# Optimization experiments

Hardware: AMD Instinct MI355X
Metric: run time of the kernel (lower is better)

The kernel has to match this reference:

```python
import jax, jax.numpy as jnp
import numpy as np

B, SQ, SK, E, H = 2, 256, 512, 512, 256

def _lin_init(k, fan_in, fan_out):
    return jax.random.normal(k, (fan_in, fan_out), jnp.float32) / np.sqrt(fan_in)

def setup_inputs() -> dict:
    key = jax.random.key(0)
    ks = jax.random.split(key, 16)
    inp = {
        'query': jax.random.normal(ks[0], (B, SQ, E), jnp.float32),
        'key':   jax.random.normal(ks[1], (B, SK, E), jnp.float32),
        # encoders
        'Wqe': _lin_init(ks[2], E, H), 'bqe': jnp.zeros((H,), jnp.float32),
        'Wke': _lin_init(ks[3], E, H), 'bke': jnp.zeros((H,), jnp.float32),
        # importance predictor: Linear(2H,H) x1, Linear(H,H) x2, Linear(H,1)
        'W0': _lin_init(ks[4], 2 * H, H), 'b0': jnp.zeros((H,), jnp.float32),
        'W1': _lin_init(ks[5], H, H),     'b1': jnp.zeros((H,), jnp.float32),
        'W2': _lin_init(ks[6], H, H),     'b2': jnp.zeros((H,), jnp.float32),
        'Wf': _lin_init(ks[7], H, 1),     'bf': jnp.zeros((1,), jnp.float32),
        # variance estimator: Linear(2H,H), Linear(H,1), Softplus
        'Wv1': _lin_init(ks[8], 2 * H, H), 'bv1': jnp.zeros((H,), jnp.float32),
        'Wv2': _lin_init(ks[9], H, 1),     'bv2': jnp.zeros((1,), jnp.float32),
    }
    return inp

def reference(query, key, Wqe, bqe, Wke, bke, W0, b0, W1, b1, W2, b2, Wf, bf, Wv1, bv1, Wv2, bv2):
    # Encoders (dropout is identity at eval): [B,Sq,H] and [B,Sk,H]
    qf = jax.nn.relu(jnp.einsum('bqe,eh->bqh', query, Wqe) + bqe)
    kf = jax.nn.relu(jnp.einsum('bke,eh->bkh', key, Wke) + bke)

    # concat([qf, kf]) @ W == qf @ W[:H] + kf @ W[H:]; avoid materializing the 2H concat
    Hd = qf.shape[-1]
    # importance predictor, layer 0 over all (q,k) pairs -> [B,Sq,Sk,H]
    q_part = jnp.einsum('bqh,hd->bqd', qf, W0[:Hd])
    k_part = jnp.einsum('bkh,hd->bkd', kf, W0[Hd:])
    h = jax.nn.relu(q_part[:, :, None, :] + k_part[:, None, :, :] + b0)
    h = jax.nn.relu(jnp.einsum('bqkh,hd->bqkd', h, W1) + b1)
    h = jax.nn.relu(jnp.einsum('bqkh,hd->bqkd', h, W2) + b2)
    importance_logits = (jnp.einsum('bqkh,ho->bqko', h, Wf) + bf)[..., 0]  # [B,Sq,Sk]

    # variance estimator
    qv = jnp.einsum('bqh,hd->bqd', qf, Wv1[:Hd])
    kv = jnp.einsum('bkh,hd->bkd', kf, Wv1[Hd:])
    v = jax.nn.relu(qv[:, :, None, :] + kv[:, None, :, :] + bv1)
    variance = jax.nn.softplus((jnp.einsum('bqkh,ho->bqko', v, Wv2) + bv2)[..., 0])

    return importance_logits, variance
```

## Files before the change

### kernel.cpp

```cpp
#include <hip/hip_runtime.h>
#include <hip/hip_bf16.h>
#include <math.h>

typedef __attribute__((ext_vector_type(4))) float f32x4;
typedef __attribute__((ext_vector_type(8))) short short8;
typedef __attribute__((ext_vector_type(4))) short short4v;

#define H_DIM 256
#define SQ_DIM 256
#define SK_DIM 512
#define E_DIM 512
#define B_DIM 2

__global__ __launch_bounds__(256) void split_cast(const float* __restrict__ query,
                                                  const float* __restrict__ key,
                                                  __hip_bfloat16* __restrict__ A1)
{
    int gid = blockIdx.x * 256 + threadIdx.x;
    int m  = gid >> 7;
    int kq = gid & 127;
    const float* src = (m < 512) ? query + (size_t)m * 512
                                 : key + (size_t)(m - 512) * 512;
    f32x4 v = *(const f32x4*)(src + kq * 4);
    short4v hv, lv;
    #pragma unroll
    for (int j = 0; j < 4; ++j) {
        __hip_bfloat16 h = __float2bfloat16(v[j]);
        float lf = v[j] - __bfloat162float(h);
        __hip_bfloat16 l = __float2bfloat16(lf);
        hv[j] = __builtin_bit_cast(short, h);
        lv[j] = __builtin_bit_cast(short, l);
    }
    *(short4v*)(A1 + (size_t)m * 1024 + kq * 4) = hv;
    *(short4v*)(A1 + (size_t)m * 1024 + 512 + kq * 4) = lv;
}

__global__ __launch_bounds__(256) void transpose_split(
    const float* __restrict__ Wqe, const float* __restrict__ Wke,
    const float* __restrict__ W0,  const float* __restrict__ Wv1,
    const float* __restrict__ W1,  const float* __restrict__ W2,
    __hip_bfloat16* __restrict__ Benc, __hip_bfloat16* __restrict__ Bproj,
    __hip_bfloat16* __restrict__ W1T,  __hip_bfloat16* __restrict__ W2T)
{
    __shared__ float tile[64][65];
    const float* S = nullptr; __hip_bfloat16* D = nullptr; int KJ = 256;
    bool split = true;
    switch (blockIdx.y) {
        case 0: S = Wqe;             D = Benc;                          KJ = 512; break;
        case 1: S = Wke;             D = Benc + 256 * 1024;             KJ = 512; break;
        case 2: S = W0;              D = Bproj;                         KJ = 256; break;
        case 3: S = Wv1;             D = Bproj + 256 * 512;             KJ = 256; break;
        case 4: S = W0 + 256 * 256;  D = Bproj + 512 * 512;             KJ = 256; break;
        case 5: S = Wv1 + 256 * 256; D = Bproj + 512 * 512 + 256 * 512; KJ = 256; break;
        case 6: S = W1;              D = W1T;  KJ = 256; split = false; break;
        case 7: S = W2;              D = W2T;  KJ = 256; split = false; break;
    }
    const int dstStride = split ? 2 * KJ : KJ;
    const int ntile = 4 * (KJ >> 6);
    const int x = blockIdx.x;
    if (x >= ntile) return;
    const int tx = x & 3, ty = x >> 2;
    const int k0 = ty * 64, n0 = tx * 64;
    const int t = threadIdx.x;
    #pragma unroll
    for (int i = 0; i < 16; ++i) {
        int r = (t >> 6) + i * 4;
        int c = t & 63;
        tile[r][c] = S[(size_t)(k0 + r) * 256 + n0 + c];
    }
    __syncthreads();
    #pragma unroll
    for (int i = 0; i < 16; ++i) {
        int r = (t >> 6) + i * 4;
        int c = t & 63;
        float v = tile[c][r];
        __hip_bfloat16 h = __float2bfloat16(v);
        D[(size_t)(n0 + r) * dstStride + k0 + c] = h;
        if (split) {
            float lf = v - __bfloat162float(h);
            D[(size_t)(n0 + r) * dstStride + KJ + k0 + c] = __float2bfloat16(lf);
        }
    }
}

template<int KD, bool SPLIT_OUT>
__global__ __launch_bounds__(256) void gemm3(
    const __hip_bfloat16* __restrict__ Apl,
    const __hip_bfloat16* __restrict__ B0,
    const __hip_bfloat16* __restrict__ B1,
    const float* __restrict__ bias0, const float* __restrict__ bias1,
    __hip_bfloat16* __restrict__ outS,
    float* __restrict__ outF0, float* __restrict__ outF1)
{
    __shared__ char smem[32768];
    const int t = threadIdx.x, lane = t & 63, wave = t >> 6;
    const int wm = wave >> 1, wn = wave & 1;
    const int m0 = blockIdx.y * 64, n0 = blockIdx.x * 64;
    const __hip_bfloat16* Arow = Apl + (size_t)m0 * (2 * KD);
    const __hip_bfloat16* Brow = ((m0 < 512) ? B0 : B1) + (size_t)n0 * (2 * KD);

    auto stage = [&](int c) {
        char* wb = smem + ((c & 1) << 14);
        const int k0 = c * 32;
        #pragma unroll
        for (int i = 0; i < 4; ++i) {
            int u = wave * 64 + lane + i * 256;
            int r = u >> 2;
            int sl = (u & 3) ^ ((r >> 1) & 3);
            int isB = r >> 7;
            int rr = r & 127;
            const __hip_bfloat16* base = isB ? Brow : Arow;
            const __hip_bfloat16* gp = base + (size_t)(rr >> 1) * (2 * KD)
                                       + (rr & 1) * KD + k0 + sl * 8;
            char* lp = wb + (wave * 64 + i * 256) * 16;
            __builtin_amdgcn_global_load_lds((const void*)gp, (void*)lp, 16, 0, 0);
        }
    };

    stage(0);
    __syncthreads();
    f32x4 acc[2][2];
    #pragma unroll
    for (int i = 0; i < 2; ++i)
        #pragma unroll
        for (int j = 0; j < 2; ++j) acc[i][j] = 0.f;

    const int NCH = KD / 32;
    for (int c = 0; c < NCH; ++c) {
        if (c + 1 < NCH) stage(c + 1);
        const char* wb = smem + ((c & 1) << 14);
        short8 ah[2], al[2];
        #pragma unroll
        for (int nt = 0; nt < 2; ++nt) {
            int n = wn * 32 + nt * 16 + (lane & 15);
            int rh = 128 + 2 * n, rl = rh + 1;
            ah[nt] = *(const short8*)(wb + rh * 64 + (((lane >> 4) ^ ((rh >> 1) & 3)) << 4));
            al[nt] = *(const short8*)(wb + rl * 64 + (((lane >> 4) ^ ((rl >> 1) & 3)) << 4));
        }
        #pragma unroll
        for (int mt = 0; mt < 2; ++mt) {
            int m = wm * 32 + mt * 16 + (lane & 15);
            int rh = 2 * m, rl = rh + 1;
            short8 bh = *(const short8*)(wb + rh * 64 + (((lane >> 4) ^ ((rh >> 1) & 3)) << 4));
            short8 bl = *(const short8*)(wb + rl * 64 + (((lane >> 4) ^ ((rl >> 1) & 3)) << 4));
            #pragma unroll
            for (int nt = 0; nt < 2; ++nt) {
                acc[mt][nt] = __builtin_amdgcn_mfma_f32_16x16x32_bf16(ah[nt], bh, acc[mt][nt], 0, 0, 0);
                acc[mt][nt] = __builtin_amdgcn_mfma_f32_16x16x32_bf16(al[nt], bh, acc[mt][nt], 0, 0, 0);
                acc[mt][nt] = __builtin_amdgcn_mfma_f32_16x16x32_bf16(ah[nt], bl, acc[mt][nt], 0, 0, 0);
            }
        }
        __syncthreads();
    }

    #pragma unroll
    for (int mt = 0; mt < 2; ++mt) {
        int m = m0 + wm * 32 + mt * 16 + (lane & 15);
        #pragma unroll
        for (int nt = 0; nt < 2; ++nt) {
            int nb = n0 + wn * 32 + nt * 16 + ((lane >> 4) << 2);
            if (SPLIT_OUT) {
                const float* bias = (m0 < 512) ? bias0 : bias1;
                f32x4 bv = *(const f32x4*)(bias + nb);
                short4v hv, lv;
                #pragma unroll
                for (int j = 0; j < 4; ++j) {
                    float v = fmaxf(acc[mt][nt][j] + bv[j], 0.f);
                    __hip_bfloat16 h = __float2bfloat16(v);
                    float lf = v - __bfloat162float(h);
                    hv[j] = __builtin_bit_cast(short, h);
                    lv[j] = __builtin_bit_cast(short, __float2bfloat16(lf));
                }
                *(short4v*)(outS + (size_t)m * 512 + nb) = hv;
                *(short4v*)(outS + (size_t)m * 512 + 256 + nb) = lv;
            } else {
                float* o = (nb < 256) ? outF0 + (size_t)m * 256 + nb
                                      : outF1 + (size_t)m * 256 + (nb - 256);
                *(f32x4*)o = acc[mt][nt];
            }
        }
    }
}

__global__ __launch_bounds__(512, 2) void pair_main(
    const float* __restrict__ qp, const float* __restrict__ kp,
    const float* __restrict__ qv, const float* __restrict__ kv,
    const __hip_bfloat16* __restrict__ W1T, const __hip_bfloat16* __restrict__ W2T,
    const float* __restrict__ b0, const float* __restrict__ b1,
    const float* __restrict__ b2, const float* __restrict__ Wf,
    const float* __restrict__ bf_, const float* __restrict__ bv1,
    const float* __restrict__ Wv2, const float* __restrict__ bv2,
    float* __restrict__ out)
{
    extern __shared__ char smem[];
    char* hbuf = smem;
    char* wbuf = smem + 65536;

    const int t    = threadIdx.x;
    const int lane = t & 63, wave = t >> 6;
    const int wm   = wave >> 2, wn = wave & 3;
    const int idx  = blockIdx.x;
    const int q    = idx >> 3;
    const int kt   = idx & 3;
    const int b    = (idx >> 2) & 1;
    const int k0g  = kt * 128;

    const float* qprow  = qp + (size_t)(b * SQ_DIM + q) * H_DIM;
    const float* kprows = kp + (size_t)(b * SK_DIM + k0g) * H_DIM;

    auto stage = [&](int g) {
        const __hip_bfloat16* Wsrc = (g < 8) ? W1T : W2T;
        const int k0 = (g & 7) * 32;
        #pragma unroll
        for (int i = 0; i < 2; ++i) {
            int u = wave * 64 + i * 512 + lane;
            int n = u >> 2;
            int s_log = (u & 3) ^ ((n >> 1) & 3);
            const __hip_bfloat16* gp = Wsrc + n * H_DIM + k0 + s_log * 8;
            char* lp = wbuf + (wave * 64 + i * 512) * 16;
            __builtin_amdgcn_global_load_lds((const void*)gp, (void*)lp, 16, 0, 0);
        }
    };

    stage(0);

    #pragma unroll
    for (int i = 0; i < 8; ++i) {
        int cidx = t + 512 * i;
        int row  = cidx >> 5;
        int c8   = cidx & 31;
        const float* kr = kprows + row * H_DIM + c8 * 8;
        f32x4 k0v = *(const f32x4*)(kr);
        f32x4 k1v = *(const f32x4*)(kr + 4);
        f32x4 q0v = *(const f32x4*)(qprow + c8 * 8);
        f32x4 q1v = *(const f32x4*)(qprow + c8 * 8 + 4);
        f32x4 z0  = *(const f32x4*)(b0 + c8 * 8);
        f32x4 z1  = *(const f32x4*)(b0 + c8 * 8 + 4);
        short8 pk;
        #pragma unroll
        for (int j = 0; j < 4; ++j) {
            float v = fmaxf(k0v[j] + q0v[j] + z0[j], 0.f);
            float w = fmaxf(k1v[j] + q1v[j] + z1[j], 0.f);
            __hip_bfloat16 hv = __float2bfloat16(v);
            __hip_bfloat16 hw = __float2bfloat16(w);
            pk[j]     = __builtin_bit_cast(short, hv);
            pk[j + 4] = __builtin_bit_cast(short, hw);
        }
        int addr = (row * 512 + c8 * 16) ^ ((row & 7) << 4);
        *(short8*)(hbuf + addr) = pk;
    }
    __syncthreads();

    f32x4 acc[4][4];
    #pragma unroll
    for (int i = 0; i < 4; ++i)
        #pragma unroll
        for (int j = 0; j < 4; ++j)
            acc[i][j] = 0.f;

    auto chunk = [&](int c, int g_next, bool do_stage) {
        short8 afrag[4];
        #pragma unroll
        for (int nt = 0; nt < 4; ++nt) {
            int n = 64 * wn + 16 * nt + (lane & 15);
            int s_lds = (lane >> 4) ^ ((n >> 1) & 3);
            afrag[nt] = *(const short8*)(wbuf + n * 64 + s_lds * 16);
        }
        __syncthreads();
        if (do_stage) stage(g_next);
        #pragma unroll
        for (int mt = 0; mt < 4; ++mt) {
            int m = 64 * wm + 16 * mt + (lane & 15);
            int addr = (m * 512 + c * 64 + ((lane >> 4) * 16)) ^ ((m & 7) << 4);
            short8 bfrag = *(const short8*)(hbuf + addr);
            #pragma unroll
            for (int nt = 0; nt < 4; ++nt)
                acc[mt][nt] = __builtin_amdgcn_mfma_f32_16x16x32_bf16(afrag[nt], bfrag, acc[mt][nt], 0, 0, 0);
        }
        __syncthreads();
    };

    for (int c = 0; c < 8; ++c)
        chunk(c, c + 1, true);

    #pragma unroll
    for (int mt = 0; mt < 4; ++mt) {
        int m = 64 * wm + 16 * mt + (lane & 15);
        #pragma unroll
        for (int nt = 0; nt < 4; ++nt) {
            int n0_ = 64 * wn + 16 * nt + ((lane >> 4) << 2);
            f32x4 bias = *(const f32x4*)(b1 + n0_);
            short4v pk;
            #pragma unroll
            for (int j = 0; j < 4; ++j) {
                float v = fmaxf(acc[mt][nt][j] + bias[j], 0.f);
                __hip_bfloat16 hv = __float2bfloat16(v);
                pk[j] = __builtin_bit_cast(short, hv);
            }
            int addr = (m * 512 + n0_ * 2) ^ ((m & 7) << 4);
            *(short4v*)(hbuf + addr) = pk;
            acc[mt][nt] = 0.f;
        }
    }
    __syncthreads();

    for (int c = 0; c < 8; ++c)
        chunk(c, 9 + c, c < 7);

    float p[4];
    #pragma unroll
    for (int mt = 0; mt < 4; ++mt) {
        float s = 0.f;
        #pragma unroll
        for (int nt = 0; nt < 4; ++nt) {
            int n0_ = 64 * wn + 16 * nt + ((lane >> 4) << 2);
            f32x4 wf   = *(const f32x4*)(Wf + n0_);
            f32x4 bias = *(const f32x4*)(b2 + n0_);
            #pragma unroll
            for (int j = 0; j < 4; ++j)
                s += fmaxf(acc[mt][nt][j] + bias[j], 0.f) * wf[j];
        }
        s += __shfl_xor(s, 16);
        s += __shfl_xor(s, 32);
        p[mt] = s;
    }

    float* lpart = (float*)smem;
    if (lane < 16) {
        #pragma unroll
        for (int mt = 0; mt < 4; ++mt)
            lpart[(wm * 64 + mt * 16 + lane) * 4 + wn] = p[mt];
    }
    __syncthreads();

    const size_t obase = (size_t)(b * SQ_DIM + q) * SK_DIM + k0g;
    if (t < 128) {
        f32x4 v = *(const f32x4*)(lpart + t * 4);
        out[obase + t] = v[0] + v[1] + v[2] + v[3] + bf_[0];
    }

    {
        int r = t >> 2, s4 = t & 3;
        const float* qvrow = qv + (size_t)(b * SQ_DIM + q) * H_DIM;
        const float* kvrow = kv + (size_t)(b * SK_DIM + k0g + r) * H_DIM;
        float a = 0.f;
        #pragma unroll
        for (int i = 0; i < 16; ++i) {
            int cidx = s4 * 64 + i * 4;
            f32x4 x  = *(const f32x4*)(qvrow + cidx);
            f32x4 y  = *(const f32x4*)(kvrow + cidx);
            f32x4 bb = *(const f32x4*)(bv1 + cidx);
            f32x4 wv = *(const f32x4*)(Wv2 + cidx);
            #pragma unroll
            for (int j = 0; j < 4; ++j)
                a += fmaxf(x[j] + y[j] + bb[j], 0.f) * wv[j];
        }
        a += __shfl_xor(a, 1);
        a += __shfl_xor(a, 2);
        if (s4 == 0) {
            float xx = a + bv2[0];
            float sp = (xx > 20.f) ? xx : log1pf(expf(xx));
            out[(size_t)B_DIM * SQ_DIM * SK_DIM + obase + r] = sp;
        }
    }
}

extern "C" void kernel_launch(void* const* d_in, const int* in_sizes, int n_in,
                              void* d_out, int out_size, void* d_ws, size_t ws_size,
                              hipStream_t stream)
{
    (void)in_sizes; (void)n_in; (void)out_size; (void)ws_size;

    const float* query = (const float*)d_in[0];
    const float* key   = (const float*)d_in[1];
    const float* Wqe   = (const float*)d_in[2];
    const float* bqe   = (const float*)d_in[3];
    const float* Wke   = (const float*)d_in[4];
    const float* bke   = (const float*)d_in[5];
    const float* W0    = (const float*)d_in[6];
    const float* b0    = (const float*)d_in[7];
    const float* W1    = (const float*)d_in[8];
    const float* b1    = (const float*)d_in[9];
    const float* W2    = (const float*)d_in[10];
    const float* b2    = (const float*)d_in[11];
    const float* Wf    = (const float*)d_in[12];
    const float* bf    = (const float*)d_in[13];
    const float* Wv1   = (const float*)d_in[14];
    const float* bv1   = (const float*)d_in[15];
    const float* Wv2   = (const float*)d_in[16];
    const float* bv2   = (const float*)d_in[17];
    float* out = (float*)d_out;

    char* ws = (char*)d_ws;
    __hip_bfloat16* A1    = (__hip_bfloat16*)(ws);
    __hip_bfloat16* Aq    = (__hip_bfloat16*)(ws + 3145728);
    __hip_bfloat16* Benc  = (__hip_bfloat16*)(ws + 4718592);
    __hip_bfloat16* Bproj = (__hip_bfloat16*)(ws + 5767168);
    __hip_bfloat16* W1T   = (__hip_bfloat16*)(ws + 6815744);
    __hip_bfloat16* W2T   = (__hip_bfloat16*)(ws + 6946816);
    float* qpkp = (float*)(ws);
    float* qvkv = (float*)(ws + 1572864);

    const float* qp = qpkp;
    const float* kp = qpkp + 512 * 256;
    const float* qv = qvkv;
    const float* kv = qvkv + 512 * 256;

    (void)hipFuncSetAttribute((const void*)pair_main,
                              hipFuncAttributeMaxDynamicSharedMemorySize, 81920);

    transpose_split<<<dim3(32, 8), 256, 0, stream>>>(Wqe, Wke, W0, Wv1, W1, W2,
                                                     Benc, Bproj, W1T, W2T);
    split_cast<<<dim3(768), 256, 0, stream>>>(query, key, A1);
    gemm3<512, true><<<dim3(4, 24), 256, 0, stream>>>(
        A1, Benc, Benc + 256 * 1024, bqe, bke, Aq, nullptr, nullptr);
    gemm3<256, false><<<dim3(8, 24), 256, 0, stream>>>(
        Aq, Bproj, Bproj + 512 * 512, nullptr, nullptr, nullptr, qpkp, qvkv);
    pair_main<<<dim3(2048), 512, 81920, stream>>>(qp, kp, qv, kv, W1T, W2T,
                                                  b0, b1, b2, Wf, bf, bv1, Wv2, bv2, out);
}
```

Before: 308.8 us.

## Load MLP weight fragments directly from global memory instead of LDS staging

After: 370.3 us. +19.9%, slower.

```diff
diff --git a/kernel.cpp b/kernel.cpp
--- a/kernel.cpp
+++ b/kernel.cpp
@@ -194,7 +194,6 @@
 {
     extern __shared__ char smem[];
     char* hbuf = smem;
-    char* wbuf = smem + 65536;
 
     const int t    = threadIdx.x;
     const int lane = t & 63, wave = t >> 6;
@@ -207,22 +206,6 @@
 
     const float* qprow  = qp + (size_t)(b * SQ_DIM + q) * H_DIM;
     const float* kprows = kp + (size_t)(b * SK_DIM + k0g) * H_DIM;
-
-    auto stage = [&](int g) {
-        const __hip_bfloat16* Wsrc = (g < 8) ? W1T : W2T;
-        const int k0 = (g & 7) * 32;
-        #pragma unroll
-        for (int i = 0; i < 2; ++i) {
-            int u = wave * 64 + i * 512 + lane;
-            int n = u >> 2;
-            int s_log = (u & 3) ^ ((n >> 1) & 3);
-            const __hip_bfloat16* gp = Wsrc + n * H_DIM + k0 + s_log * 8;
-            char* lp = wbuf + (wave * 64 + i * 512) * 16;
-            __builtin_amdgcn_global_load_lds((const void*)gp, (void*)lp, 16, 0, 0);
-        }
-    };
-
-    stage(0);
 
     #pragma unroll
     for (int i = 0; i < 8; ++i) {
@@ -258,30 +241,33 @@
         for (int j = 0; j < 4; ++j)
             acc[i][j] = 0.f;
 
-    auto chunk = [&](int c, int g_next, bool do_stage) {
-        short8 afrag[4];
-        #pragma unroll
-        for (int nt = 0; nt < 4; ++nt) {
-            int n = 64 * wn + 16 * nt + (lane & 15);
-            int s_lds = (lane >> 4) ^ ((n >> 1) & 3);
-            afrag[nt] = *(const short8*)(wbuf + n * 64 + s_lds * 16);
-        }
-        __syncthreads();
-        if (do_stage) stage(g_next);
-        #pragma unroll
-        for (int mt = 0; mt < 4; ++mt) {
-            int m = 64 * wm + 16 * mt + (lane & 15);
-            int addr = (m * 512 + c * 64 + ((lane >> 4) * 16)) ^ ((m & 7) << 4);
-            short8 bfrag = *(const short8*)(hbuf + addr);
-            #pragma unroll
-            for (int nt = 0; nt < 4; ++nt)
-                acc[mt][nt] = __builtin_amdgcn_mfma_f32_16x16x32_bf16(afrag[nt], bfrag, acc[mt][nt], 0, 0, 0);
-        }
-        __syncthreads();
+    auto gemm_layer = [&](const __hip_bfloat16* __restrict__ Wsrc) {
+        #pragma unroll
+        for (int c = 0; c < 8; ++c) {
+            short8 afrag[4], bfrag[4];
+            #pragma unroll
+            for (int nt = 0; nt < 4; ++nt) {
+                int n = 64 * wn + 16 * nt + (lane & 15);
+                afrag[nt] = *(const short8*)(Wsrc + (size_t)n * H_DIM
+                                             + c * 32 + (lane >> 4) * 8);
+            }
+            #pragma unroll
+            for (int mt = 0; mt < 4; ++mt) {
+                int m = 64 * wm + 16 * mt + (lane & 15);
+                int addr = (m * 512 + c * 64 + ((lane >> 4) * 16)) ^ ((m & 7) << 4);
+                bfrag[mt] = *(const short8*)(hbuf + addr);
+            }
+            #pragma unroll
+            for (int mt = 0; mt < 4; ++mt)
+                #pragma unroll
+                for (int nt = 0; nt < 4; ++nt)
+                    acc[mt][nt] = __builtin_amdgcn_mfma_f32_16x16x32_bf16(
+                        afrag[nt], bfrag[mt], acc[mt][nt], 0, 0, 0);
+        }
     };
 
-    for (int c = 0; c < 8; ++c)
-        chunk(c, c + 1, true);
+    gemm_layer(W1T);
+    __syncthreads();
 
     #pragma unroll
     for (int mt = 0; mt < 4; ++mt) {
@@ -304,8 +290,7 @@
     }
     __syncthreads();
 
-    for (int c = 0; c < 8; ++c)
-        chunk(c, 9 + c, c < 7);
+    gemm_layer(W2T);
 
     float p[4];
     #pragma unroll
@@ -325,6 +310,7 @@
         p[mt] = s;
     }
 
+    __syncthreads();
     float* lpart = (float*)smem;
     if (lane < 16) {
         #pragma unroll
@@ -407,7 +393,7 @@
     const float* kv = qvkv + 512 * 256;
 
     (void)hipFuncSetAttribute((const void*)pair_main,
-                              hipFuncAttributeMaxDynamicSharedMemorySize, 81920);
+                              hipFuncAttributeMaxDynamicSharedMemorySize, 65536);
 
     transpose_split<<<dim3(32, 8), 256, 0, stream>>>(Wqe, Wke, W0, Wv1, W1, W2,
                                                      Benc, Bproj, W1T, W2T);
@@ -416,6 +402,6 @@
         A1, Benc, Benc + 256 * 1024, bqe, bke, Aq, nullptr, nullptr);
     gemm3<256, false><<<dim3(8, 24), 256, 0, stream>>>(
         Aq, Bproj, Bproj + 512 * 512, nullptr, nullptr, nullptr, qpkp, qvkv);
-    pair_main<<<dim3(2048), 512, 81920, stream>>>(qp, kp, qv, kv, W1T, W2T,
+    pair_main<<<dim3(2048), 512, 65536, stream>>>(qp, kp, qv, kv, W1T, W2T,
                                                   b0, b1, b2, Wf, bf, bv1, Wv2, bv2, out);
 }
```
